# Optimization experiments

Hardware: AMD Instinct MI355X
Metric: run time of the kernel (lower is better)

Reference implementation:

```python
import jax, jax.numpy as jnp
import numpy as np


def setup_inputs() -> dict:
    key = jax.random.key(0)
    B, C, H, W = 8, 64, 64, 64
    x = jax.random.normal(key, (B, C, H, W), dtype=jnp.float32)
    return {"x": x}


def reference(x) -> jnp.ndarray:
    # x: (B, C, H, W). Spatial self-attention over N = H*W positions with
    # Q = K = V = flattened x, no scaling, no projections (the Conv2d in the
    # original __init__ is never used in forward).
    B, C, H, W = x.shape
    N = H * W
    f = x.reshape(B, C, N)  # (B, C, N)
    # att[b, n, m] = sum_c f[b, c, n] * f[b, c, m]  -> (B, N, N)
    att = jnp.einsum('bcn,bcm->bnm', f, f)
    att = jax.nn.softmax(att, axis=-1)
    # outp[b, c, n] = sum_m f[b, c, m] * att[b, n, m]^T  (f_x @ att)
    outp = jnp.einsum('bcm,bmn->bcn', f, att).reshape(B, C, H, W)
    return x + outp
```

## Files before the change

### kernel.cpp

```cpp
#include <hip/hip_runtime.h>

typedef short v8s __attribute__((ext_vector_type(8)));
typedef float v4f __attribute__((ext_vector_type(4)));

#define LOG2E 1.44269504088896340736f

#define WS_FBF_T 0u
#define WS_FVP   4194304u
#define WS_G     8388608u
#define WS_BMAX  8519680u
#define WS_TAKEN 8521728u
#define WS_NEED  8522752u

__device__ __forceinline__ unsigned short f2bf_rne(float f) {
  unsigned int u = __builtin_bit_cast(unsigned int, f);
  u += 0x7FFFu + ((u >> 16) & 1u);
  return (unsigned short)(u >> 16);
}

__device__ __forceinline__ unsigned int pack_hi16(float hi, float lo) {
#if defined(__has_builtin) && __has_builtin(__builtin_amdgcn_perm)
  return __builtin_amdgcn_perm(__builtin_bit_cast(unsigned int, hi),
                               __builtin_bit_cast(unsigned int, lo), 0x07060302u);
#else
  return (__builtin_bit_cast(unsigned int, hi) & 0xFFFF0000u) |
         (__builtin_bit_cast(unsigned int, lo) >> 16);
#endif
}

__device__ __forceinline__ int get_xcc_id() {
  return (int)(__builtin_amdgcn_s_getreg((3 << 11) | 20) & 7u);
}

__global__ __launch_bounds__(256) void prep_kernel(
    const float* __restrict__ x, unsigned short* __restrict__ fbf_t,
    unsigned short* __restrict__ fvp, float* __restrict__ g, float* __restrict__ bmax) {
  __shared__ float red[4][64];
  const int t = threadIdx.x;
  const int b = blockIdx.x & 7, ch = blockIdx.x >> 3;
  const int n0 = ch << 6, nn = t & 63, n = n0 + nn, cg = t >> 6;

  const int kin = nn & 31;
  const int slot = (kin < 16) ? (((kin >> 2) << 3) + (kin & 3))
                              : ((((kin - 16) >> 2) << 3) + ((kin - 16) & 3) + 4);
  const int ncol = (n & ~31) + slot;

  float sq = 0.f;
  unsigned short w[16];
#pragma unroll
  for (int j = 0; j < 16; ++j) {
    const int c = cg * 16 + j;
    float v = x[((size_t)(b * 64 + c) << 12) + n];
    sq = __builtin_fmaf(v, v, sq);
    w[j] = f2bf_rne(v);
  }
  unsigned short* ft = fbf_t + ((size_t)b << 18) + (size_t)n * 64 + cg * 16;
  *(v8s*)ft = *(v8s*)&w[0];
  *(v8s*)(ft + 8) = *(v8s*)&w[8];
#pragma unroll
  for (int j = 0; j < 16; ++j)
    fvp[((size_t)(b * 64 + cg * 16 + j) << 12) + ncol] = w[j];

  red[cg][nn] = sq;
  __syncthreads();
  if (t < 64) {
    float tot = (red[0][t] + red[1][t]) + (red[2][t] + red[3][t]);
    g[b * 4096 + n0 + t] = tot;
    float m = tot;
    m = fmaxf(m, __shfl_xor(m, 1, 64));
    m = fmaxf(m, __shfl_xor(m, 2, 64));
    m = fmaxf(m, __shfl_xor(m, 4, 64));
    m = fmaxf(m, __shfl_xor(m, 8, 64));
    m = fmaxf(m, __shfl_xor(m, 16, 64));
    m = fmaxf(m, __shfl_xor(m, 32, 64));
    if (t == 0) bmax[b * 64 + ch] = m;
  }
}

__global__ __launch_bounds__(512, 2) void chanattn_main(
    const float* __restrict__ x, const unsigned short* __restrict__ fbf_t,
    const unsigned short* __restrict__ fvp, const float* __restrict__ g,
    const float* __restrict__ bmax, int* __restrict__ taken,
    float* __restrict__ out) {
  __shared__ __align__(16) unsigned char smem[73728];
  unsigned short* sKtB = (unsigned short*)smem;
  unsigned short* sVcB = (unsigned short*)(smem + 18432);
  float* lred = (float*)(smem + 71680);
  const int BUF = 17920;
  __shared__ int s_tile;

  const int tid = threadIdx.x;
  const int wave = tid >> 6, lane = tid & 63, quad = lane >> 4, l15 = lane & 15;
  const int qg = wave >> 2, kg = wave & 3;

  if (tid == 0) {
    int start = (get_xcc_id() << 5);
    int t = start;
    while (atomicCAS(&taken[t], 0, 1) != 0) t = (t + 1) & 255;
    s_tile = t;
  }
  __syncthreads();
  const int tile = s_tile;
  const int b = tile >> 5, qt = tile & 31;

  const unsigned short* fT = fbf_t + ((size_t)b << 18);
  const unsigned short* fV = fvp + ((size_t)b << 18);

  const int sKey = tid >> 3, sC = (tid & 7) << 3;
  const int vC = tid >> 4, vK = (tid & 15) << 3;

  float gm = bmax[b * 64 + lane];
  gm = fmaxf(gm, __shfl_xor(gm, 1, 64));
  gm = fmaxf(gm, __shfl_xor(gm, 2, 64));
  gm = fmaxf(gm, __shfl_xor(gm, 4, 64));
  gm = fmaxf(gm, __shfl_xor(gm, 8, 64));
  gm = fmaxf(gm, __shfl_xor(gm, 16, 64));
  gm = fmaxf(gm, __shfl_xor(gm, 32, 64));
  float gq[4];
#pragma unroll
  for (int jq = 0; jq < 4; ++jq)
    gq[jq] = g[b * 4096 + qt * 128 + qg * 64 + jq * 16 + l15];

#pragma unroll
  for (int i = 0; i < 2; ++i)
    *(v8s*)&sKtB[(sKey + i * 64) * 72 + sC] =
        *(const v8s*)&fT[(size_t)(qt * 128 + sKey + i * 64) * 64 + sC];
  v8s pfk[2], pfv[2];
#pragma unroll
  for (int i = 0; i < 2; ++i)
    pfk[i] = *(const v8s*)&fT[(size_t)(sKey + i * 64) * 64 + sC];
#pragma unroll
  for (int i = 0; i < 2; ++i)
    pfv[i] = *(const v8s*)&fV[(size_t)(vC + i * 32) * 4096 + vK];

  __syncthreads();
  v8s bQ[4][2];
#pragma unroll
  for (int jq = 0; jq < 4; ++jq)
#pragma unroll
    for (int cs = 0; cs < 2; ++cs)
      bQ[jq][cs] = *(const v8s*)&sKtB[(qg * 64 + jq * 16 + l15) * 72 + cs * 32 + quad * 8];
  float msc[4];
#pragma unroll
  for (int jq = 0; jq < 4; ++jq) msc[jq] = __builtin_sqrtf(gq[jq] * gm) * LOG2E;
  __syncthreads();

#pragma unroll
  for (int i = 0; i < 2; ++i)
    *(v8s*)&sKtB[(sKey + i * 64) * 72 + sC] = pfk[i];
#pragma unroll
  for (int i = 0; i < 2; ++i)
    *(v8s*)&sVcB[(vC + i * 32) * 136 + vK] = pfv[i];
#pragma unroll
  for (int i = 0; i < 2; ++i)
    pfk[i] = *(const v8s*)&fT[(size_t)(128 + sKey + i * 64) * 64 + sC];
#pragma unroll
  for (int i = 0; i < 2; ++i)
    pfv[i] = *(const v8s*)&fV[(size_t)(vC + i * 32) * 4096 + 128 + vK];

  v4f oacc[4][4];
  float rsum[4];
#pragma unroll
  for (int ct = 0; ct < 4; ++ct)
#pragma unroll
    for (int jq = 0; jq < 4; ++jq) oacc[ct][jq] = (v4f){0.f, 0.f, 0.f, 0.f};
#pragma unroll
  for (int jq = 0; jq < 4; ++jq) rsum[jq] = 0.f;

  for (int kt = 0; kt < 32; ++kt) {
    __syncthreads();
    const int po = (kt & 1) * BUF;
    const int pn = ((kt & 1) ^ 1) * BUF;

    v8s aK[2][2];
#pragma unroll
    for (int t = 0; t < 2; ++t)
#pragma unroll
      for (int cs = 0; cs < 2; ++cs)
        aK[t][cs] =
            *(const v8s*)&sKtB[po + (kg * 32 + t * 16 + l15) * 72 + cs * 32 + quad * 8];
    v8s aV[4];
#pragma unroll
    for (int ct = 0; ct < 4; ++ct)
      aV[ct] = *(const v8s*)&sVcB[po + (ct * 16 + l15) * 136 + kg * 32 + quad * 8];

    {
      const int jq = 0;
      v4f s0 = (v4f){0.f, 0.f, 0.f, 0.f}, s1 = (v4f){0.f, 0.f, 0.f, 0.f};
#pragma unroll
      for (int cs = 0; cs < 2; ++cs) {
        s0 = __builtin_amdgcn_mfma_f32_16x16x32_bf16(aK[0][cs], bQ[jq][cs], s0, 0, 0, 0);
        s1 = __builtin_amdgcn_mfma_f32_16x16x32_bf16(aK[1][cs], bQ[jq][cs], s1, 0, 0, 0);
      }
      float p0[4], p1[4];
#pragma unroll
      for (int r = 0; r < 4; ++r) {
        p0[r] = __builtin_amdgcn_exp2f(__builtin_fmaf(s0[r], LOG2E, -msc[jq]));
        p1[r] = __builtin_amdgcn_exp2f(__builtin_fmaf(s1[r], LOG2E, -msc[jq]));
      }
      rsum[jq] += ((p0[0] + p0[1]) + (p0[2] + p0[3])) +
                  ((p1[0] + p1[1]) + (p1[2] + p1[3]));
      uint4 up;
      up.x = pack_hi16(p0[1], p0[0]);
      up.y = pack_hi16(p0[3], p0[2]);
      up.z = pack_hi16(p1[1], p1[0]);
      up.w = pack_hi16(p1[3], p1[2]);
      v8s bp = __builtin_bit_cast(v8s, up);
#pragma unroll
      for (int ct = 0; ct < 4; ++ct)
        oacc[ct][jq] =
            __builtin_amdgcn_mfma_f32_16x16x32_bf16(aV[ct], bp, oacc[ct][jq], 0, 0, 0);
    }

    if (kt < 31) {
#pragma unroll
      for (int i = 0; i < 2; ++i)
        *(v8s*)&sKtB[pn + (sKey + i * 64) * 72 + sC] = pfk[i];
#pragma unroll
      for (int i = 0; i < 2; ++i)
        *(v8s*)&sVcB[pn + (vC + i * 32) * 136 + vK] = pfv[i];
    }
    if (kt < 30) {
      const int k0 = (kt + 2) << 7;
#pragma unroll
      for (int i = 0; i < 2; ++i)
        pfk[i] = *(const v8s*)&fT[(size_t)(k0 + sKey + i * 64) * 64 + sC];
#pragma unroll
      for (int i = 0; i < 2; ++i)
        pfv[i] = *(const v8s*)&fV[(size_t)(vC + i * 32) * 4096 + k0 + vK];
    }

#pragma unroll
    for (int jq = 1; jq < 4; ++jq) {
      v4f s0 = (v4f){0.f, 0.f, 0.f, 0.f}, s1 = (v4f){0.f, 0.f, 0.f, 0.f};
#pragma unroll
      for (int cs = 0; cs < 2; ++cs) {
        s0 = __builtin_amdgcn_mfma_f32_16x16x32_bf16(aK[0][cs], bQ[jq][cs], s0, 0, 0, 0);
        s1 = __builtin_amdgcn_mfma_f32_16x16x32_bf16(aK[1][cs], bQ[jq][cs], s1, 0, 0, 0);
      }
      float p0[4], p1[4];
#pragma unroll
      for (int r = 0; r < 4; ++r) {
        p0[r] = __builtin_amdgcn_exp2f(__builtin_fmaf(s0[r], LOG2E, -msc[jq]));
        p1[r] = __builtin_amdgcn_exp2f(__builtin_fmaf(s1[r], LOG2E, -msc[jq]));
      }
      rsum[jq] += ((p0[0] + p0[1]) + (p0[2] + p0[3])) +
                  ((p1[0] + p1[1]) + (p1[2] + p1[3]));
      uint4 up;
      up.x = pack_hi16(p0[1], p0[0]);
      up.y = pack_hi16(p0[3], p0[2]);
      up.z = pack_hi16(p1[1], p1[0]);
      up.w = pack_hi16(p1[3], p1[2]);
      v8s bp = __builtin_bit_cast(v8s, up);
#pragma unroll
      for (int ct = 0; ct < 4; ++ct)
        oacc[ct][jq] =
            __builtin_amdgcn_mfma_f32_16x16x32_bf16(aV[ct], bp, oacc[ct][jq], 0, 0, 0);
    }
  }

#pragma unroll
  for (int jq = 0; jq < 4; ++jq) {
    float s = rsum[jq];
    s += __shfl_xor(s, 16, 64);
    s += __shfl_xor(s, 32, 64);
    rsum[jq] = s;
  }
  if (quad == 0) {
#pragma unroll
    for (int jq = 0; jq < 4; ++jq)
      lred[(qg * 64 + jq * 16 + l15) * 4 + kg] = rsum[jq];
  }
  __syncthreads();
  float inv[4];
#pragma unroll
  for (int jq = 0; jq < 4; ++jq) {
    const float4 lv = *(const float4*)&lred[(qg * 64 + jq * 16 + l15) * 4];
    inv[jq] = __builtin_amdgcn_rcpf((lv.x + lv.y) + (lv.z + lv.w));
  }

  float* Obuf = (float*)smem;
#pragma unroll
  for (int round = 0; round < 4; ++round) {
    if (kg == round) {
#pragma unroll
      for (int ct = 0; ct < 4; ++ct)
#pragma unroll
        for (int jq = 0; jq < 4; ++jq)
#pragma unroll
          for (int r = 0; r < 4; ++r) {
            float val = oacc[ct][jq][r] * inv[jq];
            float* p = &Obuf[(qg * 64 + ct * 16 + quad * 4 + r) * 68 + jq * 16 + l15];
            if (round == 0) *p = val; else *p += val;
          }
    }
    __syncthreads();
  }
#pragma unroll
  for (int j = 0; j < 4; ++j) {
    int idx = tid + j * 512;
    int qg2 = idx >> 10, c = (idx >> 4) & 63, q4 = idx & 15;
    const float4 o = *(const float4*)&Obuf[(qg2 * 64 + c) * 68 + q4 * 4];
    size_t gidx = ((size_t)(b * 64 + c) << 12) + (unsigned)(qt * 128 + qg2 * 64 + q4 * 4);
    const float4 xv = *(const float4*)(x + gidx);
    float4 rv;
    rv.x = xv.x + o.x; rv.y = xv.y + o.y; rv.z = xv.z + o.z; rv.w = xv.w + o.w;
    *(float4*)(out + gidx) = rv;
  }
}

__global__ __launch_bounds__(512) void
chanattn_fallback(const float* __restrict__ x, float* __restrict__ out) {
  __shared__ __align__(16) unsigned char smem[54272];
  unsigned short* sKt = (unsigned short*)smem;
  unsigned short* sVc = (unsigned short*)(smem + 18432);
  unsigned short* sP  = (unsigned short*)(smem + 35840);
  const int tid = threadIdx.x;
  const int wave = tid >> 6, lane = tid & 63, quad = lane >> 4, l15 = lane & 15;
  const int b = blockIdx.x & 7, qt = blockIdx.x >> 3;
  const float* fb = x + (size_t)b * (64 * 4096);
  const int skey = tid & 127, sc0 = (tid >> 7) << 4;
  {
    float vq[16];
#pragma unroll
    for (int j = 0; j < 16; ++j) vq[j] = fb[(sc0 + j) * 4096 + qt * 128 + skey];
    unsigned short us[16];
#pragma unroll
    for (int j = 0; j < 16; ++j) us[j] = f2bf_rne(vq[j]);
#pragma unroll
    for (int h = 0; h < 2; ++h) {
      v8s t;
#pragma unroll
      for (int j = 0; j < 8; ++j) t[j] = (short)us[h * 8 + j];
      *(v8s*)&sKt[skey * 72 + sc0 + h * 8] = t;
    }
  }
  float vk[16];
#pragma unroll
  for (int j = 0; j < 16; ++j) vk[j] = fb[(sc0 + j) * 4096 + skey];
  __syncthreads();
  v8s aq[2];
#pragma unroll
  for (int cs = 0; cs < 2; ++cs)
    aq[cs] = *(const v8s*)&sKt[(wave * 16 + l15) * 72 + cs * 32 + quad * 8];
  __syncthreads();
  v4f oacc[4];
#pragma unroll
  for (int ct = 0; ct < 4; ++ct) oacc[ct] = (v4f){0.f, 0.f, 0.f, 0.f};
  float m_run[4], l_run[4];
#pragma unroll
  for (int r = 0; r < 4; ++r) { m_run[r] = -3.0e38f; l_run[r] = 0.f; }
  unsigned short* sPw = sP + wave * (16 * 72);
  for (int kt = 0; kt < 32; ++kt) {
    {
      unsigned short us[16];
#pragma unroll
      for (int j = 0; j < 16; ++j) us[j] = f2bf_rne(vk[j]);
#pragma unroll
      for (int h = 0; h < 2; ++h) {
        v8s t;
#pragma unroll
        for (int j = 0; j < 8; ++j) t[j] = (short)us[h * 8 + j];
        *(v8s*)&sKt[skey * 72 + sc0 + h * 8] = t;
      }
#pragma unroll
      for (int j = 0; j < 16; ++j) sVc[(sc0 + j) * 136 + skey] = us[j];
    }
    __syncthreads();
    if (kt + 1 < 32) {
      const int m0 = (kt + 1) * 128;
#pragma unroll
      for (int j = 0; j < 16; ++j) vk[j] = fb[(sc0 + j) * 4096 + m0 + skey];
    }
    v4f sacc[8];
#pragma unroll
    for (int t = 0; t < 8; ++t) {
      v4f acc = (v4f){0.f, 0.f, 0.f, 0.f};
#pragma unroll
      for (int cs = 0; cs < 2; ++cs) {
        v8s bf = *(const v8s*)&sKt[(t * 16 + l15) * 72 + cs * 32 + quad * 8];
        acc = __builtin_amdgcn_mfma_f32_16x16x32_bf16(aq[cs], bf, acc, 0, 0, 0);
      }
      sacc[t] = acc;
    }
    float alpha[4], msc[4], rsum[4];
#pragma unroll
    for (int r = 0; r < 4; ++r) {
      float mv = sacc[0][r];
#pragma unroll
      for (int t = 1; t < 8; ++t) mv = fmaxf(mv, sacc[t][r]);
      mv = fmaxf(mv, __shfl_xor(mv, 8, 64));
      mv = fmaxf(mv, __shfl_xor(mv, 4, 64));
      mv = fmaxf(mv, __shfl_xor(mv, 2, 64));
      mv = fmaxf(mv, __shfl_xor(mv, 1, 64));
      float mnew = fmaxf(m_run[r], mv);
      alpha[r] = __builtin_amdgcn_exp2f((m_run[r] - mnew) * LOG2E);
      m_run[r] = mnew;
      msc[r] = mnew * LOG2E;
      l_run[r] *= alpha[r];
      rsum[r] = 0.f;
    }
#pragma unroll
    for (int ct = 0; ct < 4; ++ct)
#pragma unroll
      for (int r = 0; r < 4; ++r) oacc[ct][r] *= alpha[r];
#pragma unroll
    for (int half = 0; half < 2; ++half) {
#pragma unroll
      for (int t = half * 4; t < half * 4 + 4; ++t)
#pragma unroll
        for (int r = 0; r < 4; ++r) {
          float p = __builtin_amdgcn_exp2f(__builtin_fmaf(sacc[t][r], LOG2E, -msc[r]));
          rsum[r] += p;
          sPw[(quad * 4 + r) * 72 + (t - half * 4) * 16 + l15] = f2bf_rne(p);
        }
      asm volatile("s_waitcnt lgkmcnt(0)" ::: "memory");
#pragma unroll
      for (int ms = 0; ms < 2; ++ms) {
        v8s af = *(const v8s*)&sPw[l15 * 72 + ms * 32 + quad * 8];
#pragma unroll
        for (int ct = 0; ct < 4; ++ct) {
          v8s bf = *(const v8s*)&sVc[(ct * 16 + l15) * 136 + (half * 2 + ms) * 32 + quad * 8];
          oacc[ct] = __builtin_amdgcn_mfma_f32_16x16x32_bf16(af, bf, oacc[ct], 0, 0, 0);
        }
      }
      asm volatile("s_waitcnt lgkmcnt(0)" ::: "memory");
    }
#pragma unroll
    for (int r = 0; r < 4; ++r) {
      float s = rsum[r];
      s += __shfl_xor(s, 8, 64);
      s += __shfl_xor(s, 4, 64);
      s += __shfl_xor(s, 2, 64);
      s += __shfl_xor(s, 1, 64);
      l_run[r] += s;
    }
    __syncthreads();
  }
  float inv[4];
#pragma unroll
  for (int r = 0; r < 4; ++r) inv[r] = __builtin_amdgcn_rcpf(l_run[r]);
  float* sOt = (float*)smem;
#pragma unroll
  for (int ct = 0; ct < 4; ++ct)
#pragma unroll
    for (int r = 0; r < 4; ++r)
      sOt[(ct * 16 + l15) * 132 + wave * 16 + quad * 4 + r] = oacc[ct][r] * inv[r];
  __syncthreads();
#pragma unroll
  for (int j = 0; j < 4; ++j) {
    int idx = tid + j * 512;
    int nv = idx & 31, c = idx >> 5;
    float4 o = *(const float4*)&sOt[c * 132 + nv * 4];
    size_t gaddr = (size_t)b * (64 * 4096) + (size_t)c * 4096 + (size_t)(qt * 128 + nv * 4);
    float4 xv = *(const float4*)(x + gaddr);
    float4 res = make_float4(xv.x + o.x, xv.y + o.y, xv.z + o.z, xv.w + o.w);
    *(float4*)(out + gaddr) = res;
  }
}

extern "C" void kernel_launch(void* const* d_in, const int* in_sizes, int n_in,
                              void* d_out, int out_size, void* d_ws, size_t ws_size,
                              hipStream_t stream) {
  const float* xin = (const float*)d_in[0];
  float* out = (float*)d_out;
  if (ws_size >= (size_t)WS_NEED) {
    unsigned short* fbf_t = (unsigned short*)((char*)d_ws + WS_FBF_T);
    unsigned short* fvp = (unsigned short*)((char*)d_ws + WS_FVP);
    float* g = (float*)((char*)d_ws + WS_G);
    float* bmax = (float*)((char*)d_ws + WS_BMAX);
    int* taken = (int*)((char*)d_ws + WS_TAKEN);
    hipMemsetAsync(taken, 0, 256 * sizeof(int), stream);
    prep_kernel<<<dim3(512), dim3(256), 0, stream>>>(xin, fbf_t, fvp, g, bmax);
    chanattn_main<<<dim3(256), dim3(512), 0, stream>>>(xin, fbf_t, fvp, g, bmax, taken, out);
  } else {
    chanattn_fallback<<<dim3(256), dim3(512), 0, stream>>>(xin, out);
  }
}
```

Baseline: 117.0 us.

## Split key range across blocks with atomic partial outputs and separate normalization kernel

Replaces the atomic tile scheduler with a split-K decomposition. Each block now handles 256 queries over half of the keys, giving each wave four query subtiles per key chunk for more K/V reuse. Unnormalized partial outputs are accumulated into the zeroed output with float atomicAdd, and the row sums go to workspace. A new final_norm kernel then divides by the summed row sums and adds the residual. The cost is an extra memset, an extra kernel launch, atomic traffic to global memory, and a re-read of the output, while dropping the XCD-aware tile claiming. It also relies on the shared per-batch max so the two halves can be combined without rescaling.

New measurement: 125.3 us. 1.07x slower.

```diff
diff --git a/kernel.cpp b/kernel.cpp
--- a/kernel.cpp
+++ b/kernel.cpp
@@ -9,8 +9,8 @@
 #define WS_FVP   4194304u
 #define WS_G     8388608u
 #define WS_BMAX  8519680u
-#define WS_TAKEN 8521728u
-#define WS_NEED  8522752u
+#define WS_LSUM  8521728u
+#define WS_NEED  8783872u
 
 __device__ __forceinline__ unsigned short f2bf_rne(float f) {
   unsigned int u = __builtin_bit_cast(unsigned int, f);
@@ -26,10 +26,6 @@
   return (__builtin_bit_cast(unsigned int, hi) & 0xFFFF0000u) |
          (__builtin_bit_cast(unsigned int, lo) >> 16);
 #endif
-}
-
-__device__ __forceinline__ int get_xcc_id() {
-  return (int)(__builtin_amdgcn_s_getreg((3 << 11) | 20) & 7u);
 }
 
 __global__ __launch_bounds__(256) void prep_kernel(
@@ -78,30 +74,20 @@
 }
 
 __global__ __launch_bounds__(512, 2) void chanattn_main(
-    const float* __restrict__ x, const unsigned short* __restrict__ fbf_t,
-    const unsigned short* __restrict__ fvp, const float* __restrict__ g,
-    const float* __restrict__ bmax, int* __restrict__ taken,
-    float* __restrict__ out) {
+    const unsigned short* __restrict__ fbf_t, const unsigned short* __restrict__ fvp,
+    const float* __restrict__ g, const float* __restrict__ bmax,
+    float* __restrict__ lws, float* __restrict__ out) {
   __shared__ __align__(16) unsigned char smem[73728];
   unsigned short* sKtB = (unsigned short*)smem;
   unsigned short* sVcB = (unsigned short*)(smem + 18432);
   float* lred = (float*)(smem + 71680);
   const int BUF = 17920;
-  __shared__ int s_tile;
 
   const int tid = threadIdx.x;
   const int wave = tid >> 6, lane = tid & 63, quad = lane >> 4, l15 = lane & 15;
-  const int qg = wave >> 2, kg = wave & 3;
-
-  if (tid == 0) {
-    int start = (get_xcc_id() << 5);
-    int t = start;
-    while (atomicCAS(&taken[t], 0, 1) != 0) t = (t + 1) & 255;
-    s_tile = t;
-  }
-  __syncthreads();
-  const int tile = s_tile;
-  const int b = tile >> 5, qt = tile & 31;
+  const int qg = wave >> 1, kg = wave & 1;
+  const int b = blockIdx.x & 7, qt = (blockIdx.x >> 3) & 15, sp = blockIdx.x >> 7;
+  const int k00 = sp << 11;
 
   const unsigned short* fT = fbf_t + ((size_t)b << 18);
   const unsigned short* fV = fvp + ((size_t)b << 18);
@@ -119,27 +105,32 @@
   float gq[4];
 #pragma unroll
   for (int jq = 0; jq < 4; ++jq)
-    gq[jq] = g[b * 4096 + qt * 128 + qg * 64 + jq * 16 + l15];
-
-#pragma unroll
-  for (int i = 0; i < 2; ++i)
-    *(v8s*)&sKtB[(sKey + i * 64) * 72 + sC] =
-        *(const v8s*)&fT[(size_t)(qt * 128 + sKey + i * 64) * 64 + sC];
+    gq[jq] = g[b * 4096 + qt * 256 + qg * 64 + jq * 16 + l15];
+
+#pragma unroll
+  for (int i = 0; i < 4; ++i) {
+    int row = sKey + i * 64;
+    *(v8s*)&sKtB[(row >> 7) * BUF + (row & 127) * 72 + sC] =
+        *(const v8s*)&fT[(size_t)(qt * 256 + row) * 64 + sC];
+  }
   v8s pfk[2], pfv[2];
 #pragma unroll
   for (int i = 0; i < 2; ++i)
-    pfk[i] = *(const v8s*)&fT[(size_t)(sKey + i * 64) * 64 + sC];
-#pragma unroll
-  for (int i = 0; i < 2; ++i)
-    pfv[i] = *(const v8s*)&fV[(size_t)(vC + i * 32) * 4096 + vK];
+    pfk[i] = *(const v8s*)&fT[(size_t)(k00 + sKey + i * 64) * 64 + sC];
+#pragma unroll
+  for (int i = 0; i < 2; ++i)
+    pfv[i] = *(const v8s*)&fV[(size_t)(vC + i * 32) * 4096 + k00 + vK];
 
   __syncthreads();
   v8s bQ[4][2];
 #pragma unroll
-  for (int jq = 0; jq < 4; ++jq)
+  for (int jq = 0; jq < 4; ++jq) {
+    int row = qg * 64 + jq * 16 + l15;
 #pragma unroll
     for (int cs = 0; cs < 2; ++cs)
-      bQ[jq][cs] = *(const v8s*)&sKtB[(qg * 64 + jq * 16 + l15) * 72 + cs * 32 + quad * 8];
+      bQ[jq][cs] =
+          *(const v8s*)&sKtB[(row >> 7) * BUF + (row & 127) * 72 + cs * 32 + quad * 8];
+  }
   float msc[4];
 #pragma unroll
   for (int jq = 0; jq < 4; ++jq) msc[jq] = __builtin_sqrtf(gq[jq] * gm) * LOG2E;
@@ -153,44 +144,49 @@
     *(v8s*)&sVcB[(vC + i * 32) * 136 + vK] = pfv[i];
 #pragma unroll
   for (int i = 0; i < 2; ++i)
-    pfk[i] = *(const v8s*)&fT[(size_t)(128 + sKey + i * 64) * 64 + sC];
-#pragma unroll
-  for (int i = 0; i < 2; ++i)
-    pfv[i] = *(const v8s*)&fV[(size_t)(vC + i * 32) * 4096 + 128 + vK];
+    pfk[i] = *(const v8s*)&fT[(size_t)(k00 + 128 + sKey + i * 64) * 64 + sC];
+#pragma unroll
+  for (int i = 0; i < 2; ++i)
+    pfv[i] = *(const v8s*)&fV[(size_t)(vC + i * 32) * 4096 + k00 + 128 + vK];
 
   v4f oacc[4][4];
   float rsum[4];
 #pragma unroll
-  for (int ct = 0; ct < 4; ++ct)
-#pragma unroll
-    for (int jq = 0; jq < 4; ++jq) oacc[ct][jq] = (v4f){0.f, 0.f, 0.f, 0.f};
-#pragma unroll
-  for (int jq = 0; jq < 4; ++jq) rsum[jq] = 0.f;
-
-  for (int kt = 0; kt < 32; ++kt) {
+  for (int jq = 0; jq < 4; ++jq) {
+    rsum[jq] = 0.f;
+#pragma unroll
+    for (int ct = 0; ct < 4; ++ct) oacc[jq][ct] = (v4f){0.f, 0.f, 0.f, 0.f};
+  }
+
+  for (int kt = 0; kt < 16; ++kt) {
     __syncthreads();
     const int po = (kt & 1) * BUF;
     const int pn = ((kt & 1) ^ 1) * BUF;
 
-    v8s aK[2][2];
-#pragma unroll
-    for (int t = 0; t < 2; ++t)
-#pragma unroll
-      for (int cs = 0; cs < 2; ++cs)
-        aK[t][cs] =
-            *(const v8s*)&sKtB[po + (kg * 32 + t * 16 + l15) * 72 + cs * 32 + quad * 8];
-    v8s aV[4];
-#pragma unroll
-    for (int ct = 0; ct < 4; ++ct)
-      aV[ct] = *(const v8s*)&sVcB[po + (ct * 16 + l15) * 136 + kg * 32 + quad * 8];
-
-    {
-      const int jq = 0;
+    v8s aK[2][2][2];
+#pragma unroll
+    for (int ch = 0; ch < 2; ++ch)
+#pragma unroll
+      for (int t = 0; t < 2; ++t)
+#pragma unroll
+        for (int cs = 0; cs < 2; ++cs)
+          aK[ch][t][cs] = *(const v8s*)&sKtB[po + (kg * 64 + ch * 32 + t * 16 + l15) * 72 +
+                                             cs * 32 + quad * 8];
+    v8s aV[2][4];
+#pragma unroll
+    for (int ch = 0; ch < 2; ++ch)
+#pragma unroll
+      for (int ct = 0; ct < 4; ++ct)
+        aV[ch][ct] = *(const v8s*)&sVcB[po + (ct * 16 + l15) * 136 + kg * 64 + ch * 32 +
+                                        quad * 8];
+
+#pragma unroll
+    for (int jq = 0; jq < 4; ++jq) {
       v4f s0 = (v4f){0.f, 0.f, 0.f, 0.f}, s1 = (v4f){0.f, 0.f, 0.f, 0.f};
 #pragma unroll
       for (int cs = 0; cs < 2; ++cs) {
-        s0 = __builtin_amdgcn_mfma_f32_16x16x32_bf16(aK[0][cs], bQ[jq][cs], s0, 0, 0, 0);
-        s1 = __builtin_amdgcn_mfma_f32_16x16x32_bf16(aK[1][cs], bQ[jq][cs], s1, 0, 0, 0);
+        s0 = __builtin_amdgcn_mfma_f32_16x16x32_bf16(aK[0][0][cs], bQ[jq][cs], s0, 0, 0, 0);
+        s1 = __builtin_amdgcn_mfma_f32_16x16x32_bf16(aK[0][1][cs], bQ[jq][cs], s1, 0, 0, 0);
       }
       float p0[4], p1[4];
 #pragma unroll
@@ -208,11 +204,11 @@
       v8s bp = __builtin_bit_cast(v8s, up);
 #pragma unroll
       for (int ct = 0; ct < 4; ++ct)
-        oacc[ct][jq] =
-            __builtin_amdgcn_mfma_f32_16x16x32_bf16(aV[ct], bp, oacc[ct][jq], 0, 0, 0);
-    }
-
-    if (kt < 31) {
+        oacc[jq][ct] =
+            __builtin_amdgcn_mfma_f32_16x16x32_bf16(aV[0][ct], bp, oacc[jq][ct], 0, 0, 0);
+    }
+
+    if (kt < 15) {
 #pragma unroll
       for (int i = 0; i < 2; ++i)
         *(v8s*)&sKtB[pn + (sKey + i * 64) * 72 + sC] = pfk[i];
@@ -220,8 +216,8 @@
       for (int i = 0; i < 2; ++i)
         *(v8s*)&sVcB[pn + (vC + i * 32) * 136 + vK] = pfv[i];
     }
-    if (kt < 30) {
-      const int k0 = (kt + 2) << 7;
+    if (kt < 14) {
+      const int k0 = k00 + ((kt + 2) << 7);
 #pragma unroll
       for (int i = 0; i < 2; ++i)
         pfk[i] = *(const v8s*)&fT[(size_t)(k0 + sKey + i * 64) * 64 + sC];
@@ -231,12 +227,12 @@
     }
 
 #pragma unroll
-    for (int jq = 1; jq < 4; ++jq) {
+    for (int jq = 0; jq < 4; ++jq) {
       v4f s0 = (v4f){0.f, 0.f, 0.f, 0.f}, s1 = (v4f){0.f, 0.f, 0.f, 0.f};
 #pragma unroll
       for (int cs = 0; cs < 2; ++cs) {
-        s0 = __builtin_amdgcn_mfma_f32_16x16x32_bf16(aK[0][cs], bQ[jq][cs], s0, 0, 0, 0);
-        s1 = __builtin_amdgcn_mfma_f32_16x16x32_bf16(aK[1][cs], bQ[jq][cs], s1, 0, 0, 0);
+        s0 = __builtin_amdgcn_mfma_f32_16x16x32_bf16(aK[1][0][cs], bQ[jq][cs], s0, 0, 0, 0);
+        s1 = __builtin_amdgcn_mfma_f32_16x16x32_bf16(aK[1][1][cs], bQ[jq][cs], s1, 0, 0, 0);
       }
       float p0[4], p1[4];
 #pragma unroll
@@ -254,8 +250,8 @@
       v8s bp = __builtin_bit_cast(v8s, up);
 #pragma unroll
       for (int ct = 0; ct < 4; ++ct)
-        oacc[ct][jq] =
-            __builtin_amdgcn_mfma_f32_16x16x32_bf16(aV[ct], bp, oacc[ct][jq], 0, 0, 0);
+        oacc[jq][ct] =
+            __builtin_amdgcn_mfma_f32_16x16x32_bf16(aV[1][ct], bp, oacc[jq][ct], 0, 0, 0);
     }
   }
 
@@ -266,45 +262,63 @@
     s += __shfl_xor(s, 32, 64);
     rsum[jq] = s;
   }
+  __syncthreads();
   if (quad == 0) {
 #pragma unroll
     for (int jq = 0; jq < 4; ++jq)
-      lred[(qg * 64 + jq * 16 + l15) * 4 + kg] = rsum[jq];
-  }
-  __syncthreads();
-  float inv[4];
-#pragma unroll
-  for (int jq = 0; jq < 4; ++jq) {
-    const float4 lv = *(const float4*)&lred[(qg * 64 + jq * 16 + l15) * 4];
-    inv[jq] = __builtin_amdgcn_rcpf((lv.x + lv.y) + (lv.z + lv.w));
+      lred[((qg * 4 + jq) * 16 + l15) * 2 + kg] = rsum[jq];
+  }
+  __syncthreads();
+  if (kg == 0 && quad == 0) {
+#pragma unroll
+    for (int jq = 0; jq < 4; ++jq) {
+      int i = (qg * 4 + jq) * 16 + l15;
+      lws[sp * 32768 + b * 4096 + qt * 256 + i] = lred[i * 2] + lred[i * 2 + 1];
+    }
   }
 
   float* Obuf = (float*)smem;
 #pragma unroll
-  for (int round = 0; round < 4; ++round) {
+  for (int round = 0; round < 2; ++round) {
     if (kg == round) {
 #pragma unroll
-      for (int ct = 0; ct < 4; ++ct)
-#pragma unroll
-        for (int jq = 0; jq < 4; ++jq)
+      for (int jq = 0; jq < 4; ++jq)
+#pragma unroll
+        for (int ct = 0; ct < 4; ++ct)
 #pragma unroll
           for (int r = 0; r < 4; ++r) {
-            float val = oacc[ct][jq][r] * inv[jq];
-            float* p = &Obuf[(qg * 64 + ct * 16 + quad * 4 + r) * 68 + jq * 16 + l15];
-            if (round == 0) *p = val; else *p += val;
+            float* p = &Obuf[(ct * 16 + quad * 4 + r) * 257 + qg * 64 + jq * 16 + l15];
+            if (round == 0) *p = oacc[jq][ct][r]; else *p += oacc[jq][ct][r];
           }
     }
     __syncthreads();
   }
 #pragma unroll
-  for (int j = 0; j < 4; ++j) {
-    int idx = tid + j * 512;
-    int qg2 = idx >> 10, c = (idx >> 4) & 63, q4 = idx & 15;
-    const float4 o = *(const float4*)&Obuf[(qg2 * 64 + c) * 68 + q4 * 4];
-    size_t gidx = ((size_t)(b * 64 + c) << 12) + (unsigned)(qt * 128 + qg2 * 64 + q4 * 4);
-    const float4 xv = *(const float4*)(x + gidx);
+  for (int k = 0; k < 32; ++k) {
+    int idx = tid + k * 512;
+    int c = idx >> 8, q = idx & 255;
+    atomicAdd(out + ((size_t)(b * 64 + c) << 12) + qt * 256 + q, Obuf[c * 257 + q]);
+  }
+}
+
+__global__ __launch_bounds__(256) void final_norm(
+    const float* __restrict__ x, const float* __restrict__ lws, float* __restrict__ out) {
+  const int b = blockIdx.x & 7, seg = blockIdx.x >> 3;
+  const int t = threadIdx.x;
+#pragma unroll
+  for (int j = 0; j < 8; ++j) {
+    int fl = seg * 2048 + j * 256 + t;
+    int c = fl >> 10, n4 = (fl & 1023) << 2;
+    size_t gidx = ((size_t)(b * 64 + c) << 12) + n4;
+    float4 o = *(const float4*)(out + gidx);
+    float4 xv = *(const float4*)(x + gidx);
+    float4 l0 = *(const float4*)(lws + b * 4096 + n4);
+    float4 l1 = *(const float4*)(lws + 32768 + b * 4096 + n4);
     float4 rv;
-    rv.x = xv.x + o.x; rv.y = xv.y + o.y; rv.z = xv.z + o.z; rv.w = xv.w + o.w;
+    rv.x = xv.x + o.x * __builtin_amdgcn_rcpf(l0.x + l1.x);
+    rv.y = xv.y + o.y * __builtin_amdgcn_rcpf(l0.y + l1.y);
+    rv.z = xv.z + o.z * __builtin_amdgcn_rcpf(l0.z + l1.z);
+    rv.w = xv.w + o.w * __builtin_amdgcn_rcpf(l0.w + l1.w);
     *(float4*)(out + gidx) = rv;
   }
 }
@@ -469,10 +483,11 @@
     unsigned short* fvp = (unsigned short*)((char*)d_ws + WS_FVP);
     float* g = (float*)((char*)d_ws + WS_G);
     float* bmax = (float*)((char*)d_ws + WS_BMAX);
-    int* taken = (int*)((char*)d_ws + WS_TAKEN);
-    hipMemsetAsync(taken, 0, 256 * sizeof(int), stream);
+    float* lws = (float*)((char*)d_ws + WS_LSUM);
+    hipMemsetAsync(d_out, 0, (size_t)out_size * sizeof(float), stream);
     prep_kernel<<<dim3(512), dim3(256), 0, stream>>>(xin, fbf_t, fvp, g, bmax);
-    chanattn_main<<<dim3(256), dim3(512), 0, stream>>>(xin, fbf_t, fvp, g, bmax, taken, out);
+    chanattn_main<<<dim3(256), dim3(512), 0, stream>>>(fbf_t, fvp, g, bmax, lws, out);
+    final_norm<<<dim3(256), dim3(256), 0, stream>>>(xin, lws, out);
   } else {
     chanattn_fallback<<<dim3(256), dim3(512), 0, stream>>>(xin, out);
   }
```
